# Optimization experiments

Measured on AMD Instinct MI355X. Metric: run time of the kernel, lower is better.

## Reference

```python
import jax, jax.numpy as jnp
import numpy as np
import math

B, S, D, H, FF = 8, 1024, 1024, 16, 4096
DH = D // H
EPS = 1e-5


def _layernorm(x, g, b):
    mu = jnp.mean(x, axis=-1, keepdims=True)
    var = jnp.mean((x - mu) ** 2, axis=-1, keepdims=True)
    return (x - mu) * jax.lax.rsqrt(var + EPS) * g + b


def _gelu_tanh(x):
    c = math.sqrt(2.0 / math.pi)
    return 0.5 * x * (1.0 + jnp.tanh(c * (x + 0.044715 * x ** 3)))


def setup_inputs() -> dict:
    key = jax.random.key(0)
    ks = jax.random.split(key, 8)
    s = lambda d: 1.0 / math.sqrt(d)
    return {
        "x": jax.random.normal(ks[0], (B, S, D), jnp.float32),
        "ln1_g": jnp.ones((D,), jnp.float32),
        "ln1_b": jnp.zeros((D,), jnp.float32),
        "w_qkv": jax.random.normal(ks[1], (3 * D, D), jnp.float32) * s(D),
        "b_qkv": jax.random.normal(ks[2], (3 * D,), jnp.float32) * 0.02,
        "w_o": jax.random.normal(ks[3], (D, D), jnp.float32) * s(D),
        "b_o": jax.random.normal(ks[4], (D,), jnp.float32) * 0.02,
        "ln2_g": jnp.ones((D,), jnp.float32),
        "ln2_b": jnp.zeros((D,), jnp.float32),
        "w1": jax.random.normal(ks[5], (FF, D), jnp.float32) * s(D),
        "b1": jax.random.normal(ks[6], (FF,), jnp.float32) * 0.02,
        "w2": jax.random.normal(ks[7], (D, FF), jnp.float32) * s(FF),
        "b2": jnp.zeros((D,), jnp.float32),
    }


def reference(x, ln1_g, ln1_b, w_qkv, b_qkv, w_o, b_o, ln2_g, ln2_b, w1, b1, w2, b2):
    # --- pre-LN causal self-attention ---
    h = _layernorm(x, ln1_g, ln1_b)
    qkv = h @ w_qkv.T + b_qkv                      # [B,S,3D]
    q, k, v = jnp.split(qkv, 3, axis=-1)
    q = q.reshape(B, S, H, DH)
    k = k.reshape(B, S, H, DH)
    v = v.reshape(B, S, H, DH)
    scores = jnp.einsum("bqhd,bkhd->bhqk", q, k) / math.sqrt(DH)
    causal = jnp.triu(jnp.ones((S, S), jnp.bool_), 1)  # True above diagonal
    scores = jnp.where(causal, -jnp.inf, scores)
    attn = jax.nn.softmax(scores, axis=-1)
    o = jnp.einsum("bhqk,bkhd->bqhd", attn, v).reshape(B, S, D)
    x = x + (o @ w_o.T + b_o)
    # --- FFN ---
    h = _layernorm(x, ln2_g, ln2_b)
    h = _gelu_tanh(h @ w1.T + b1) @ w2.T + b2
    return x + h
```

## Files before the change

### kernel.cpp

```cpp
#include <hip/hip_runtime.h>
#include <math.h>


typedef __bf16 bf16_t;
typedef __bf16 bf16x4 __attribute__((ext_vector_type(4)));
typedef __bf16 bf16x8 __attribute__((ext_vector_type(8)));
typedef float f32x4 __attribute__((ext_vector_type(4)));

#define WAITVM(N) asm volatile("s_waitcnt vmcnt(" #N ")" ::: "memory")
#define WAITLGKM0 asm volatile("s_waitcnt lgkmcnt(0)" ::: "memory")
#define SCHEDBAR __builtin_amdgcn_sched_barrier(0)

__device__ __forceinline__ void async16(const void* g, void* l) {
    __builtin_amdgcn_global_load_lds(
        (const __attribute__((address_space(1))) void*)g,
        (__attribute__((address_space(3))) void*)l,
        16, 0, 0);
}

__device__ __forceinline__ void ln_row(const float* __restrict__ x,
                                       const float* __restrict__ g,
                                       const float* __restrict__ bb,
                                       bf16_t* __restrict__ out, int row) {
    const int tid = threadIdx.x;
    const float4 xv = *(const float4*)(x + row * 1024 + tid * 4);
    float s1 = xv.x + xv.y + xv.z + xv.w;
    float s2 = xv.x * xv.x + xv.y * xv.y + xv.z * xv.z + xv.w * xv.w;
#pragma unroll
    for (int m = 32; m >= 1; m >>= 1) {
        s1 += __shfl_xor(s1, m);
        s2 += __shfl_xor(s2, m);
    }
    __shared__ float r1[4], r2[4];
    const int wid = tid >> 6, lane = tid & 63;
    if (lane == 0) { r1[wid] = s1; r2[wid] = s2; }
    __syncthreads();
    s1 = r1[0] + r1[1] + r1[2] + r1[3];
    s2 = r2[0] + r2[1] + r2[2] + r2[3];
    const float mu = s1 * (1.0f / 1024.0f);
    const float var = s2 * (1.0f / 1024.0f) - mu * mu;
    const float rs = rsqrtf(var + 1e-5f);
    const float4 gv = *(const float4*)(g + tid * 4);
    const float4 bv = *(const float4*)(bb + tid * 4);
    bf16x4 o;
    o[0] = (bf16_t)((xv.x - mu) * rs * gv.x + bv.x);
    o[1] = (bf16_t)((xv.y - mu) * rs * gv.y + bv.y);
    o[2] = (bf16_t)((xv.z - mu) * rs * gv.z + bv.z);
    o[3] = (bf16_t)((xv.w - mu) * rs * gv.w + bv.w);
    *(bf16x4*)(out + row * 1024 + tid * 4) = o;
}

__global__ __launch_bounds__(256) void prep(
    const float* __restrict__ s0, const float* __restrict__ s1,
    const float* __restrict__ s2, const float* __restrict__ s3,
    bf16_t* __restrict__ d0, bf16_t* __restrict__ d1,
    bf16_t* __restrict__ d2, bf16_t* __restrict__ d3,
    const float* __restrict__ x, const float* __restrict__ ln1g,
    const float* __restrict__ ln1b, bf16_t* __restrict__ h) {
    if (blockIdx.x >= 12288) {
        ln_row(x, ln1g, ln1b, h, blockIdx.x - 12288);
        return;
    }
    const int g = blockIdx.x * 256 + threadIdx.x;
    const float* s;
    bf16_t* d;
    int off;
    if (g < 786432)       { s = s0; d = d0; off = g; }
    else if (g < 1048576) { s = s1; d = d1; off = g - 786432; }
    else if (g < 2097152) { s = s2; d = d2; off = g - 1048576; }
    else                  { s = s3; d = d3; off = g - 2097152; }
    const int i = off * 4;
    const float4 v = *(const float4*)(s + i);
    bf16x4 o;
    o[0] = (bf16_t)v.x; o[1] = (bf16_t)v.y; o[2] = (bf16_t)v.z; o[3] = (bf16_t)v.w;
    *(bf16x4*)(d + i) = o;
}

__global__ __launch_bounds__(256) void ln_b(const bf16_t* __restrict__ x,
                                            const float* __restrict__ g,
                                            const float* __restrict__ bb,
                                            bf16_t* __restrict__ out) {
    const int tid = threadIdx.x;
    const int row = blockIdx.x;
    const bf16x4 xb = *(const bf16x4*)(x + row * 1024 + tid * 4);
    const float x0 = (float)xb[0], x1 = (float)xb[1], x2 = (float)xb[2], x3 = (float)xb[3];
    float s1 = x0 + x1 + x2 + x3;
    float s2 = x0 * x0 + x1 * x1 + x2 * x2 + x3 * x3;
#pragma unroll
    for (int m = 32; m >= 1; m >>= 1) {
        s1 += __shfl_xor(s1, m);
        s2 += __shfl_xor(s2, m);
    }
    __shared__ float r1[4], r2[4];
    const int wid = tid >> 6, lane = tid & 63;
    if (lane == 0) { r1[wid] = s1; r2[wid] = s2; }
    __syncthreads();
    s1 = r1[0] + r1[1] + r1[2] + r1[3];
    s2 = r2[0] + r2[1] + r2[2] + r2[3];
    const float mu = s1 * (1.0f / 1024.0f);
    const float var = s2 * (1.0f / 1024.0f) - mu * mu;
    const float rs = rsqrtf(var + 1e-5f);
    const float4 gv = *(const float4*)(g + tid * 4);
    const float4 bv = *(const float4*)(bb + tid * 4);
    bf16x4 o;
    o[0] = (bf16_t)((x0 - mu) * rs * gv.x + bv.x);
    o[1] = (bf16_t)((x1 - mu) * rs * gv.y + bv.y);
    o[2] = (bf16_t)((x2 - mu) * rs * gv.z + bv.z);
    o[3] = (bf16_t)((x3 - mu) * rs * gv.w + bv.w);
    *(bf16x4*)(out + row * 1024 + tid * 4) = o;
}

template <int MODE>
__global__ __launch_bounds__(256, 2) void gemm_bt(
    const bf16_t* __restrict__ A, const bf16_t* __restrict__ W,
    const float* __restrict__ bias, const float* __restrict__ residf,
    const bf16_t* __restrict__ residb,
    bf16_t* __restrict__ outb, float* __restrict__ outf,
    bf16_t* __restrict__ vt, int N, int K) {
    __shared__ bf16_t As[128 * 64];
    __shared__ bf16_t Bs[128 * 64];
    const int tid = threadIdx.x;
    const int w = tid >> 6;
    const int lane = tid & 63;
    const int l15 = lane & 15;
    const int quad = lane >> 4;

    const int nbn = N >> 7;
    const int per = 8 * nbn;
    const int lid = blockIdx.x;
    const int bm = (lid / per) * 8 + (lid % per) % 8;
    const int bn = (lid % per) / 8;
    const int m0 = bm * 128;
    const int n0 = bn * 128;
    const int wm = (w & 1) * 64;
    const int wn = (w >> 1) * 64;

    int rr[4], so[4];
#pragma unroll
    for (int q = 0; q < 4; q++) {
        const int c = q * 256 + w * 64 + lane;
        rr[q] = c >> 3;
        so[q] = ((c & 7) ^ (rr[q] & 7)) * 8;
    }
    const bf16_t* pA[4];
    const bf16_t* pB[4];
#pragma unroll
    for (int q = 0; q < 4; q++) {
        pA[q] = A + (size_t)(m0 + rr[q]) * K + so[q];
        pB[q] = W + (size_t)(n0 + rr[q]) * K + so[q];
    }

    f32x4 acc[4][4] = {};

    for (int k0 = 0; k0 < K; k0 += 64) {
#pragma unroll
        for (int q = 0; q < 4; q++) {
            async16(pA[q], As + q * 2048 + w * 512);
            async16(pB[q], Bs + q * 2048 + w * 512);
            pA[q] += 64; pB[q] += 64;
        }
        __syncthreads();

        bf16x8 af[4][2], bfr[4][2];
#pragma unroll
        for (int i = 0; i < 4; i++) {
            const int r = wm + i * 16 + l15;
#pragma unroll
            for (int f = 0; f < 2; f++) {
                const int slot = (f * 4 + quad) ^ (r & 7);
                af[i][f] = *(const bf16x8*)(As + r * 64 + slot * 8);
            }
        }
#pragma unroll
        for (int j = 0; j < 4; j++) {
            const int r = wn + j * 16 + l15;
#pragma unroll
            for (int f = 0; f < 2; f++) {
                const int slot = (f * 4 + quad) ^ (r & 7);
                bfr[j][f] = *(const bf16x8*)(Bs + r * 64 + slot * 8);
            }
        }
#pragma unroll
        for (int i = 0; i < 4; i++)
#pragma unroll
            for (int j = 0; j < 4; j++)
#pragma unroll
                for (int f = 0; f < 2; f++)
                    acc[i][j] = __builtin_amdgcn_mfma_f32_16x16x32_bf16(
                        af[i][f], bfr[j][f], acc[i][j], 0, 0, 0);
        __syncthreads();
    }

#pragma unroll
    for (int i = 0; i < 4; i++) {
#pragma unroll
        for (int j = 0; j < 4; j++) {
            const int col = n0 + wn + j * 16 + l15;
            const float bcol = bias[col];
            const int row0 = m0 + wm + i * 16 + quad * 4;
            float v4[4];
#pragma unroll
            for (int q = 0; q < 4; q++) {
                float v = acc[i][j][q] + bcol;
                if (MODE == 1) {
                    const float u2 = -1.5957691216057308f * (v + 0.044715f * v * v * v);
                    v = v * __builtin_amdgcn_rcpf(1.0f + __expf(u2));
                }
                v4[q] = v;
            }
            if (MODE == 4) {
#pragma unroll
                for (int q = 0; q < 4; q++) {
                    const size_t idx = (size_t)(row0 + q) * N + col;
                    outb[idx] = (bf16_t)(v4[q] + residf[idx]);
                }
            } else if (MODE == 5) {
#pragma unroll
                for (int q = 0; q < 4; q++) {
                    const size_t idx = (size_t)(row0 + q) * N + col;
                    outf[idx] = v4[q] + (float)residb[idx];
                }
            } else if (MODE == 3 && col >= 2048) {
                const int bh = (row0 >> 10) * 16 + ((col - 2048) >> 6);
                const int d = (col - 2048) & 63;
                bf16x4 pk;
#pragma unroll
                for (int q = 0; q < 4; q++) pk[q] = (bf16_t)v4[q];
                *(bf16x4*)(vt + (size_t)bh * 65536 + d * 1024 + (row0 & 1023)) = pk;
            } else {
#pragma unroll
                for (int q = 0; q < 4; q++)
                    outb[(size_t)(row0 + q) * N + col] = (bf16_t)v4[q];
            }
        }
    }
}

template <int MODE>
__global__ __launch_bounds__(512, 2) void gemm8(
    const bf16_t* __restrict__ A, const bf16_t* __restrict__ W,
    const float* __restrict__ bias, bf16_t* __restrict__ outb,
    bf16_t* __restrict__ vt, int N, int K) {
    __shared__ bf16_t lds[65536];
    const int tid = threadIdx.x;
    const int w = tid >> 6, lane = tid & 63;
    const int l15 = lane & 15, quad = lane >> 4;
    const int wr = w >> 2, wc = w & 3;

    const int nwg = gridDim.x;
    const int wg = (blockIdx.x & 7) * (nwg >> 3) + (blockIdx.x >> 3);
    const int nbn = N >> 8;
    const int per = 8 * nbn;
    const int bm = (wg / per) * 8 + (wg % per) % 8;
    const int bn = (wg % per) / 8;
    const int m0 = bm << 8, n0 = bn << 8;

    int r_[2], s_[2];
#pragma unroll
    for (int L = 0; L < 2; L++) {
        const int c = L * 512 + tid;
        r_[L] = c >> 3;
        s_[L] = ((c & 7) ^ (r_[L] & 7)) * 8;
    }
    const bf16_t* pa0[2]; const bf16_t* pa1[2];
    const bf16_t* pb0[2]; const bf16_t* pb1[2];
#pragma unroll
    for (int L = 0; L < 2; L++) {
        pa0[L] = A + (size_t)(m0 + r_[L]) * K + s_[L];
        pa1[L] = pa0[L] + (size_t)128 * K;
        pb0[L] = W + (size_t)(n0 + r_[L]) * K + s_[L];
        pb1[L] = pb0[L] + (size_t)128 * K;
    }

    const int swz0 = (quad ^ (l15 & 7)) * 8;
    const int swz1 = ((4 + quad) ^ (l15 & 7)) * 8;
    const bf16_t* bA0 = lds + wr * 4096 + l15 * 64 + swz0;
    const bf16_t* bA1 = lds + wr * 4096 + l15 * 64 + swz1;
    const bf16_t* bB0 = lds + 16384 + wc * 2048 + l15 * 64 + swz0;
    const bf16_t* bB1 = lds + 16384 + wc * 2048 + l15 * 64 + swz1;
    const bf16_t* cA0 = bA0 + 32768;
    const bf16_t* cA1 = bA1 + 32768;
    const bf16_t* cB0 = bB0 + 32768;
    const bf16_t* cB1 = bB1 + 32768;

    f32x4 acc[8][4] = {};
    bf16x8 af[4][2], bfr[4][2];

    async16(pa0[0], lds + w * 512);
    async16(pa0[1], lds + 4096 + w * 512);
    async16(pb0[0], lds + 16384 + w * 512);
    async16(pb0[1], lds + 20480 + w * 512);
    async16(pb1[0], lds + 24576 + w * 512);
    async16(pb1[1], lds + 28672 + w * 512);
    async16(pa1[0], lds + 8192 + w * 512);
    async16(pa1[1], lds + 12288 + w * 512);
    WAITVM(0);
    __builtin_amdgcn_s_barrier();

    const int NT = K >> 6;
    int p = 0;
    for (int t = 0; t < NT; ++t, p ^= 1) {
        bf16_t* nb = lds + (p ^ 1) * 32768;
        const int kn = (t + 1) << 6;

#pragma unroll
        for (int i = 0; i < 4; i++) {
            af[i][0] = *(const bf16x8*)(bA0 + i * 1024);
            af[i][1] = *(const bf16x8*)(bA1 + i * 1024);
        }
#pragma unroll
        for (int j = 0; j < 2; j++) {
            bfr[j][0] = *(const bf16x8*)(bB0 + j * 1024);
            bfr[j][1] = *(const bf16x8*)(bB1 + j * 1024);
        }
        if (t + 1 < NT) {
            async16(pa0[0] + kn, nb + w * 512);
            async16(pa0[1] + kn, nb + 4096 + w * 512);
            async16(pb0[0] + kn, nb + 16384 + w * 512);
            async16(pb0[1] + kn, nb + 20480 + w * 512);
            async16(pb1[0] + kn, nb + 24576 + w * 512);
            async16(pb1[1] + kn, nb + 28672 + w * 512);
            async16(pa1[0] + kn, nb + 8192 + w * 512);
            async16(pa1[1] + kn, nb + 12288 + w * 512);
        }
        SCHEDBAR;
        __builtin_amdgcn_s_barrier();
        WAITLGKM0;
        SCHEDBAR;
        __builtin_amdgcn_s_setprio(1);
#pragma unroll
        for (int i = 0; i < 4; i++)
#pragma unroll
            for (int j = 0; j < 2; j++)
#pragma unroll
                for (int f = 0; f < 2; f++)
                    acc[i][j] = __builtin_amdgcn_mfma_f32_16x16x32_bf16(af[i][f], bfr[j][f], acc[i][j], 0, 0, 0);
        __builtin_amdgcn_s_setprio(0);
        SCHEDBAR;
        __builtin_amdgcn_s_barrier();

#pragma unroll
        for (int j = 2; j < 4; j++) {
            bfr[j][0] = *(const bf16x8*)(bB0 + 8192 + (j & 1) * 1024);
            bfr[j][1] = *(const bf16x8*)(bB1 + 8192 + (j & 1) * 1024);
        }
        SCHEDBAR;
        __builtin_amdgcn_s_barrier();
        WAITLGKM0;
        SCHEDBAR;
        __builtin_amdgcn_s_setprio(1);
#pragma unroll
        for (int i = 0; i < 4; i++)
#pragma unroll
            for (int j = 2; j < 4; j++)
#pragma unroll
                for (int f = 0; f < 2; f++)
                    acc[i][j] = __builtin_amdgcn_mfma_f32_16x16x32_bf16(af[i][f], bfr[j][f], acc[i][j], 0, 0, 0);
        __builtin_amdgcn_s_setprio(0);
        SCHEDBAR;
        __builtin_amdgcn_s_barrier();

#pragma unroll
        for (int i = 0; i < 4; i++) {
            af[i][0] = *(const bf16x8*)(bA0 + 8192 + i * 1024);
            af[i][1] = *(const bf16x8*)(bA1 + 8192 + i * 1024);
        }
        SCHEDBAR;
        __builtin_amdgcn_s_barrier();
        WAITLGKM0;
        SCHEDBAR;
        __builtin_amdgcn_s_setprio(1);
#pragma unroll
        for (int i = 0; i < 4; i++)
#pragma unroll
            for (int j = 0; j < 2; j++)
#pragma unroll
                for (int f = 0; f < 2; f++)
                    acc[i + 4][j] = __builtin_amdgcn_mfma_f32_16x16x32_bf16(af[i][f], bfr[j][f], acc[i + 4][j], 0, 0, 0);
        __builtin_amdgcn_s_setprio(0);
        SCHEDBAR;
        __builtin_amdgcn_s_barrier();

        __builtin_amdgcn_s_setprio(1);
#pragma unroll
        for (int i = 0; i < 4; i++)
#pragma unroll
            for (int j = 2; j < 4; j++)
#pragma unroll
                for (int f = 0; f < 2; f++)
                    acc[i + 4][j] = __builtin_amdgcn_mfma_f32_16x16x32_bf16(af[i][f], bfr[j][f], acc[i + 4][j], 0, 0, 0);
        __builtin_amdgcn_s_setprio(0);
        SCHEDBAR;
        WAITVM(0);
        __builtin_amdgcn_s_barrier();

        { const bf16_t* s;
          s = bA0; bA0 = cA0; cA0 = s;
          s = bA1; bA1 = cA1; cA1 = s;
          s = bB0; bB0 = cB0; cB0 = s;
          s = bB1; bB1 = cB1; cB1 = s; }
    }

#pragma unroll
    for (int i = 0; i < 8; i++) {
        const int row0 = m0 + (i >> 2) * 128 + wr * 64 + (i & 3) * 16 + quad * 4;
#pragma unroll
        for (int j = 0; j < 4; j++) {
            const int col = n0 + (j >> 1) * 128 + wc * 32 + (j & 1) * 16 + l15;
            const float bcol = bias[col];
            float v4[4];
#pragma unroll
            for (int q = 0; q < 4; q++) {
                float v = acc[i][j][q] + bcol;
                if (MODE == 1) {
                    const float u2 = -1.5957691216057308f * (v + 0.044715f * v * v * v);
                    v = v * __builtin_amdgcn_rcpf(1.0f + __expf(u2));
                }
                v4[q] = v;
            }
            if (MODE == 3 && col >= 2048) {
                const int bh = (row0 >> 10) * 16 + ((col - 2048) >> 6);
                const int d = (col - 2048) & 63;
                bf16x4 pk;
#pragma unroll
                for (int q = 0; q < 4; q++) pk[q] = (bf16_t)v4[q];
                *(bf16x4*)(vt + (size_t)bh * 65536 + d * 1024 + (row0 & 1023)) = pk;
            } else {
#pragma unroll
                for (int q = 0; q < 4; q++)
                    outb[(size_t)(row0 + q) * N + col] = (bf16_t)v4[q];
            }
        }
    }
}

__global__ __launch_bounds__(512) void attn_mfma(const bf16_t* __restrict__ qkv,
                                                 const bf16_t* __restrict__ vt,
                                                 bf16_t* __restrict__ o) {
    __shared__ bf16_t Ks[4096];
    __shared__ bf16_t Vs[4096];
    __shared__ bf16_t Ps[8][32][72];
    const int tid = threadIdx.x;
    const int w = tid >> 6;
    const int lane = tid & 63;
    const int l15 = lane & 15;
    const int quad = lane >> 4;
    const int qb = blockIdx.x;
    const int bh = blockIdx.y;
    const int b = bh >> 4, h = bh & 15;

    const int qrow = b * 1024 + qb * 256 + w * 32;

    bf16x8 qf[2][2];
#pragma unroll
    for (int g = 0; g < 2; g++)
#pragma unroll
        for (int f = 0; f < 2; f++) {
            bf16x8 t = *(const bf16x8*)(qkv + (size_t)(qrow + g * 16 + l15) * 3072 + h * 64 + f * 32 + quad * 8);
#pragma unroll
            for (int e = 0; e < 8; e++) t[e] = (bf16_t)((float)t[e] * 0.125f);
            qf[g][f] = t;
        }

    f32x4 Ot[2][4] = {};
    float mrow[2] = {-3.0e38f, -3.0e38f};
    float lrow[2] = {0.0f, 0.0f};

    const int c0 = w * 64 + lane;
    const int r0 = c0 >> 3, g0 = (((c0 & 7) ^ (r0 & 7))) * 8;

    const bf16_t* kbase = qkv + (size_t)(b * 1024) * 3072 + 1024 + h * 64;
    const bf16_t* vbase = vt + (size_t)bh * 64 * 1024;

    const int ktmax = 4 * qb + 3;
    for (int kt = 0; kt <= ktmax; kt++) {
        async16(kbase + (size_t)(kt * 64 + r0) * 3072 + g0, Ks + w * 512);
        async16(vbase + (size_t)r0 * 1024 + kt * 64 + g0, Vs + w * 512);
        __syncthreads();

#pragma unroll
        for (int g = 0; g < 2; g++) {
            const int qmaxw = qb * 256 + w * 32 + g * 16 + 15;
            if (kt * 64 > qmaxw) continue;
            const int ktd = qmaxw >> 6;
            const int kbd = (2 * w + g) & 3;

            f32x4 sf[4];
#pragma unroll
            for (int kb = 0; kb < 4; kb++) {
                if (kt * 64 + kb * 16 > qmaxw) {
                    sf[kb] = (f32x4){-3.0e38f, -3.0e38f, -3.0e38f, -3.0e38f};
                    continue;
                }
                const int r = kb * 16 + l15;
                f32x4 acc = {};
#pragma unroll
                for (int f = 0; f < 2; f++) {
                    const int seg = (f * 4 + quad) ^ (r & 7);
                    const bf16x8 kf = *(const bf16x8*)(Ks + r * 64 + seg * 8);
                    acc = __builtin_amdgcn_mfma_f32_16x16x32_bf16(kf, qf[g][f], acc, 0, 0, 0);
                }
                if (kt == ktd && kb == kbd) {
#pragma unroll
                    for (int rr2 = 0; rr2 < 4; rr2++)
                        if (quad * 4 + rr2 > l15) acc[rr2] = -3.0e38f;
                }
                sf[kb] = acc;
            }

            float tmax = -3.0e38f;
#pragma unroll
            for (int kb = 0; kb < 4; kb++)
#pragma unroll
                for (int rr2 = 0; rr2 < 4; rr2++) tmax = fmaxf(tmax, sf[kb][rr2]);
            tmax = fmaxf(tmax, __shfl_xor(tmax, 16));
            tmax = fmaxf(tmax, __shfl_xor(tmax, 32));
            const float mnew = fmaxf(mrow[g], tmax);
            const float alpha = __expf(mrow[g] - mnew);
            float psum = 0.0f;
#pragma unroll
            for (int kb = 0; kb < 4; kb++) {
                bf16x4 pk;
#pragma unroll
                for (int rr2 = 0; rr2 < 4; rr2++) {
                    const float p = __expf(sf[kb][rr2] - mnew);
                    psum += p;
                    pk[rr2] = (bf16_t)p;
                }
                *(bf16x4*)(&Ps[w][g * 16 + l15][kb * 16 + quad * 4]) = pk;
            }
            psum += __shfl_xor(psum, 16);
            psum += __shfl_xor(psum, 32);
            lrow[g] = lrow[g] * alpha + psum;
            mrow[g] = mnew;
#pragma unroll
            for (int db = 0; db < 4; db++)
#pragma unroll
                for (int rr2 = 0; rr2 < 4; rr2++) Ot[g][db][rr2] *= alpha;

#pragma unroll
            for (int ks = 0; ks < 2; ks++) {
                if (kt * 64 + ks * 32 > qmaxw) break;
                const bf16x8 pf = *(const bf16x8*)(&Ps[w][g * 16 + l15][ks * 32 + quad * 8]);
#pragma unroll
                for (int db = 0; db < 4; db++) {
                    const int d = db * 16 + l15;
                    const int seg = (ks * 4 + quad) ^ (d & 7);
                    const bf16x8 vf = *(const bf16x8*)(Vs + d * 64 + seg * 8);
                    Ot[g][db] = __builtin_amdgcn_mfma_f32_16x16x32_bf16(vf, pf, Ot[g][db], 0, 0, 0);
                }
            }
        }
        __syncthreads();
    }

#pragma unroll
    for (int g = 0; g < 2; g++) {
        const float rl = 1.0f / lrow[g];
#pragma unroll
        for (int db = 0; db < 4; db++) {
            bf16x4 ov;
#pragma unroll
            for (int rr2 = 0; rr2 < 4; rr2++) ov[rr2] = (bf16_t)(Ot[g][db][rr2] * rl);
            *(bf16x4*)(o + (size_t)(qrow + g * 16 + l15) * 1024 + h * 64 + db * 16 + quad * 4) = ov;
        }
    }
}

extern "C" void kernel_launch(void* const* d_in, const int* in_sizes, int n_in,
                              void* d_out, int out_size, void* d_ws, size_t ws_size,
                              hipStream_t stream) {
    const float* x     = (const float*)d_in[0];
    const float* ln1g  = (const float*)d_in[1];
    const float* ln1b  = (const float*)d_in[2];
    const float* w_qkv = (const float*)d_in[3];
    const float* b_qkv = (const float*)d_in[4];
    const float* w_o   = (const float*)d_in[5];
    const float* b_o   = (const float*)d_in[6];
    const float* ln2g  = (const float*)d_in[7];
    const float* ln2b  = (const float*)d_in[8];
    const float* w1    = (const float*)d_in[9];
    const float* b1    = (const float*)d_in[10];
    const float* w2    = (const float*)d_in[11];
    const float* b2    = (const float*)d_in[12];
    float* out = (float*)d_out;

    char* w = (char*)d_ws;
    bf16_t* wbqkv = (bf16_t*)(w + 0);
    bf16_t* wbo   = (bf16_t*)(w + 6291456);
    bf16_t* wb1   = (bf16_t*)(w + 8388608);
    bf16_t* wb2   = (bf16_t*)(w + 16777216);
    bf16_t* h     = (bf16_t*)(w + 25165824);
    bf16_t* qkv   = (bf16_t*)(w + 41943040);
    bf16_t* ob    = (bf16_t*)(w + 92274688);
    bf16_t* x1b   = (bf16_t*)(w + 109051904);
    bf16_t* f     = (bf16_t*)(w + 142606336);
    bf16_t* vtb   = (bf16_t*)(w + 142606336);

    prep<<<20480, 256, 0, stream>>>(w_qkv, w_o, w1, w2, wbqkv, wbo, wb1, wb2,
                                    x, ln1g, ln1b, h);
    gemm8<3><<<384, 512, 0, stream>>>(h, wbqkv, b_qkv, qkv, vtb, 3072, 1024);
    attn_mfma<<<dim3(4, 128), 512, 0, stream>>>(qkv, vtb, ob);
    gemm_bt<4><<<64 * 8, 256, 0, stream>>>(ob, wbo, b_o, x, nullptr, x1b, nullptr, nullptr, 1024, 1024);
    ln_b<<<8192, 256, 0, stream>>>(x1b, ln2g, ln2b, h);
    gemm8<1><<<512, 512, 0, stream>>>(h, wb1, b1, f, nullptr, 4096, 1024);
    gemm_bt<5><<<64 * 8, 256, 0, stream>>>(f, wb2, b2, nullptr, x1b, nullptr, out, nullptr, 1024, 4096);
}
```

Baseline: 451.0 us.

## Stagger GEMM async prefetches across sub-phases with partial vmcnt waits and peeled tail

Instead of issuing all eight async global-to-LDS loads for the next K tile at once and draining them with a full vmcnt(0) wait, the loads are spread in pairs across the four MFMA sub-phases. Each barrier waits only on the quarter of the next tile that is needed, using vmcnt(4). The last iteration is peeled out so the steady-state loop needs no bounds check, and the next buffer pointer is taken from the swapped fragment pointers. This aims to overlap global memory latency with MFMA work more finely, at the cost of more delicate wait-count bookkeeping that could hide races if miscounted.

```diff
diff --git a/kernel.cpp b/kernel.cpp
--- a/kernel.cpp
+++ b/kernel.cpp
@@ -272,10 +272,11 @@
         pb1[L] = pb0[L] + (size_t)128 * K;
     }
 
+    const int fragoff = wr * 4096 + l15 * 64;
     const int swz0 = (quad ^ (l15 & 7)) * 8;
     const int swz1 = ((4 + quad) ^ (l15 & 7)) * 8;
-    const bf16_t* bA0 = lds + wr * 4096 + l15 * 64 + swz0;
-    const bf16_t* bA1 = lds + wr * 4096 + l15 * 64 + swz1;
+    const bf16_t* bA0 = lds + fragoff + swz0;
+    const bf16_t* bA1 = lds + fragoff + swz1;
     const bf16_t* bB0 = lds + 16384 + wc * 2048 + l15 * 64 + swz0;
     const bf16_t* bB1 = lds + 16384 + wc * 2048 + l15 * 64 + swz1;
     const bf16_t* cA0 = bA0 + 32768;
@@ -294,13 +295,12 @@
     async16(pb1[1], lds + 28672 + w * 512);
     async16(pa1[0], lds + 8192 + w * 512);
     async16(pa1[1], lds + 12288 + w * 512);
-    WAITVM(0);
+    WAITVM(4);
     __builtin_amdgcn_s_barrier();
 
     const int NT = K >> 6;
-    int p = 0;
-    for (int t = 0; t < NT; ++t, p ^= 1) {
-        bf16_t* nb = lds + (p ^ 1) * 32768;
+    for (int t = 0; t < NT - 1; ++t) {
+        bf16_t* nb = (bf16_t*)(cA0 - (fragoff + swz0));
         const int kn = (t + 1) << 6;
 
 #pragma unroll
@@ -313,16 +313,8 @@
             bfr[j][0] = *(const bf16x8*)(bB0 + j * 1024);
             bfr[j][1] = *(const bf16x8*)(bB1 + j * 1024);
         }
-        if (t + 1 < NT) {
-            async16(pa0[0] + kn, nb + w * 512);
-            async16(pa0[1] + kn, nb + 4096 + w * 512);
-            async16(pb0[0] + kn, nb + 16384 + w * 512);
-            async16(pb0[1] + kn, nb + 20480 + w * 512);
-            async16(pb1[0] + kn, nb + 24576 + w * 512);
-            async16(pb1[1] + kn, nb + 28672 + w * 512);
-            async16(pa1[0] + kn, nb + 8192 + w * 512);
-            async16(pa1[1] + kn, nb + 12288 + w * 512);
-        }
+        async16(pa0[0] + kn, nb + w * 512);
+        async16(pa0[1] + kn, nb + 4096 + w * 512);
         SCHEDBAR;
         __builtin_amdgcn_s_barrier();
         WAITLGKM0;
@@ -337,6 +329,7 @@
                     acc[i][j] = __builtin_amdgcn_mfma_f32_16x16x32_bf16(af[i][f], bfr[j][f], acc[i][j], 0, 0, 0);
         __builtin_amdgcn_s_setprio(0);
         SCHEDBAR;
+        WAITVM(4);
         __builtin_amdgcn_s_barrier();
 
 #pragma unroll
@@ -344,6 +337,8 @@
             bfr[j][0] = *(const bf16x8*)(bB0 + 8192 + (j & 1) * 1024);
             bfr[j][1] = *(const bf16x8*)(bB1 + 8192 + (j & 1) * 1024);
         }
+        async16(pb0[0] + kn, nb + 16384 + w * 512);
+        async16(pb0[1] + kn, nb + 20480 + w * 512);
         SCHEDBAR;
         __builtin_amdgcn_s_barrier();
         WAITLGKM0;
@@ -358,6 +353,7 @@
                     acc[i][j] = __builtin_amdgcn_mfma_f32_16x16x32_bf16(af[i][f], bfr[j][f], acc[i][j], 0, 0, 0);
         __builtin_amdgcn_s_setprio(0);
         SCHEDBAR;
+        WAITVM(4);
         __builtin_amdgcn_s_barrier();
 
 #pragma unroll
@@ -365,6 +361,8 @@
             af[i][0] = *(const bf16x8*)(bA0 + 8192 + i * 1024);
             af[i][1] = *(const bf16x8*)(bA1 + 8192 + i * 1024);
         }
+        async16(pb1[0] + kn, nb + 24576 + w * 512);
+        async16(pb1[1] + kn, nb + 28672 + w * 512);
         SCHEDBAR;
         __builtin_amdgcn_s_barrier();
         WAITLGKM0;
@@ -381,6 +379,9 @@
         SCHEDBAR;
         __builtin_amdgcn_s_barrier();
 
+        async16(pa1[0] + kn, nb + 8192 + w * 512);
+        async16(pa1[1] + kn, nb + 12288 + w * 512);
+        SCHEDBAR;
         __builtin_amdgcn_s_setprio(1);
 #pragma unroll
         for (int i = 0; i < 4; i++)
@@ -391,7 +392,7 @@
                     acc[i + 4][j] = __builtin_amdgcn_mfma_f32_16x16x32_bf16(af[i][f], bfr[j][f], acc[i + 4][j], 0, 0, 0);
         __builtin_amdgcn_s_setprio(0);
         SCHEDBAR;
-        WAITVM(0);
+        WAITVM(4);
         __builtin_amdgcn_s_barrier();
 
         { const bf16_t* s;
@@ -399,6 +400,72 @@
           s = bA1; bA1 = cA1; cA1 = s;
           s = bB0; bB0 = cB0; cB0 = s;
           s = bB1; bB1 = cB1; cB1 = s; }
+    }
+
+    {
+#pragma unroll
+        for (int i = 0; i < 4; i++) {
+            af[i][0] = *(const bf16x8*)(bA0 + i * 1024);
+            af[i][1] = *(const bf16x8*)(bA1 + i * 1024);
+        }
+#pragma unroll
+        for (int j = 0; j < 2; j++) {
+            bfr[j][0] = *(const bf16x8*)(bB0 + j * 1024);
+            bfr[j][1] = *(const bf16x8*)(bB1 + j * 1024);
+        }
+        SCHEDBAR;
+        __builtin_amdgcn_s_barrier();
+        WAITLGKM0;
+        SCHEDBAR;
+        __builtin_amdgcn_s_setprio(1);
+#pragma unroll
+        for (int i = 0; i < 4; i++)
+#pragma unroll
+            for (int j = 0; j < 2; j++)
+#pragma unroll
+                for (int f = 0; f < 2; f++)
+                    acc[i][j] = __builtin_amdgcn_mfma_f32_16x16x32_bf16(af[i][f], bfr[j][f], acc[i][j], 0, 0, 0);
+        __builtin_amdgcn_s_setprio(0);
+        SCHEDBAR;
+        WAITVM(2);
+        __builtin_amdgcn_s_barrier();
+#pragma unroll
+        for (int j = 2; j < 4; j++) {
+            bfr[j][0] = *(const bf16x8*)(bB0 + 8192 + (j & 1) * 1024);
+            bfr[j][1] = *(const bf16x8*)(bB1 + 8192 + (j & 1) * 1024);
+        }
+        SCHEDBAR;
+        __builtin_amdgcn_s_barrier();
+        WAITLGKM0;
+        SCHEDBAR;
+        __builtin_amdgcn_s_setprio(1);
+#pragma unroll
+        for (int i = 0; i < 4; i++)
+#pragma unroll
+            for (int j = 2; j < 4; j++)
+#pragma unroll
+                for (int f = 0; f < 2; f++)
+                    acc[i][j] = __builtin_amdgcn_mfma_f32_16x16x32_bf16(af[i][f], bfr[j][f], acc[i][j], 0, 0, 0);
+        __builtin_amdgcn_s_setprio(0);
+        SCHEDBAR;
+        WAITVM(0);
+        __builtin_amdgcn_s_barrier();
+#pragma unroll
+        for (int i = 0; i < 4; i++) {
+            af[i][0] = *(const bf16x8*)(bA0 + 8192 + i * 1024);
+            af[i][1] = *(const bf16x8*)(bA1 + 8192 + i * 1024);
+        }
+        WAITLGKM0;
+        SCHEDBAR;
+        __builtin_amdgcn_s_setprio(1);
+#pragma unroll
+        for (int i = 0; i < 4; i++)
+#pragma unroll
+            for (int j = 0; j < 4; j++)
+#pragma unroll
+                for (int f = 0; f < 2; f++)
+                    acc[i + 4][j] = __builtin_amdgcn_mfma_f32_16x16x32_bf16(af[i][f], bfr[j][f], acc[i + 4][j], 0, 0, 0);
+        __builtin_amdgcn_s_setprio(0);
     }
 
 #pragma unroll
```

New measurement: 436.2 us. 3.3% less time.
